# Kernel tuning notes

Measured on AMD Instinct MI355X. Metric: run time of the kernel, lower is better.

The kernel has to match this reference:

```python
import jax, jax.numpy as jnp
import numpy as np

B, C = 32768, 1000
ALPHA, P, BETA = 0.5, 2.0, 0.3
E1, E2 = 60, 80
MAGIC = 0.165745444183859  # constant subtracted from max_m in __init__


def setup_inputs() -> dict:
    key = jax.random.key(0)
    k1, k2, k3, k4 = jax.random.split(key, 4)
    x = jax.random.normal(k1, (B, C), dtype=jnp.float32)
    targets = jax.random.randint(k2, (B,), 0, C)
    # per-class sample counts (long-tailed): positive floats in [5, 1280]
    cls_num_list = jax.random.uniform(k3, (C,), dtype=jnp.float32, minval=5.0, maxval=1280.0)
    class_difficulty = jax.random.uniform(k4, (C,), dtype=jnp.float32)
    return {"x": x, "targets": targets, "cls_num_list": cls_num_list,
            "class_difficulty": class_difficulty, "epoch": 70}


def reference(x, targets, cls_num_list, class_difficulty, epoch):
    # ---- margins from class frequency (computed in __init__) ----
    max_m = -jnp.log(jnp.min(cls_num_list) / jnp.sum(cls_num_list)) - MAGIC
    cls_p = 1.0 / jnp.sqrt(cls_num_list)          # [C]
    m_list = max_m * cls_p / jnp.max(cls_p)       # [C]
    # ---- difficulty-based weights ----
    weights = ALPHA * class_difficulty ** P + BETA
    weights = weights * (max_m / jnp.max(weights))
    # ---- epoch schedule (epoch is a static Python int) ----
    if epoch < E1:
        m_list1 = m_list
    else:
        ee = 1.0 if epoch >= E2 else (epoch - E1) / (E2 - E1)
        m_list1 = m_list + weights * ee / 2
    # ---- subtract per-sample margin only at the target logit ----
    batch_m = m_list1[targets]                    # [B], == matmul(m_list1, onehot.T)
    rows = jnp.arange(B)
    output = x.at[rows, targets].add(-batch_m)    # torch.where(index, x - batch_m, x)
    # ---- safe_cross_entropy with s=1.0 (s kwarg not passed at call site) ----
    log_probs = jax.nn.log_softmax(output * 1.0, axis=1)
    loss = -jnp.mean(log_probs[rows, targets])
    return loss
```

## Files before the change

### kernel.cpp

```cpp
#include <hip/hip_runtime.h>
#include <math.h>

#define B_SZ 32768
#define C_SZ 1000
#define NV4  250

typedef float fvec4 __attribute__((ext_vector_type(4)));

__constant__ float kMAGIC = 0.165745444183859f;

__global__ void prep_kernel(const float* __restrict__ cls,
                            const float* __restrict__ diff,
                            const int*   __restrict__ epoch_p,
                            float*       __restrict__ m1) {
    __shared__ float smin[256], ssum[256], smax[256];
    const int tid = threadIdx.x;
    float mn = INFINITY, sm = 0.f, mx = -INFINITY;
    for (int c = tid; c < C_SZ; c += 256) {
        float v = cls[c];
        mn = fminf(mn, v);
        sm += v;
        mx = fmaxf(mx, diff[c]);
    }
    smin[tid] = mn; ssum[tid] = sm; smax[tid] = mx;
    __syncthreads();
    for (int s = 128; s > 0; s >>= 1) {
        if (tid < s) {
            smin[tid] = fminf(smin[tid], smin[tid + s]);
            ssum[tid] += ssum[tid + s];
            smax[tid] = fmaxf(smax[tid], smax[tid + s]);
        }
        __syncthreads();
    }
    __shared__ float sh_maxm, sh_minc, sh_wsc, sh_ee2;
    if (tid == 0) {
        const float minc = smin[0], sumc = ssum[0], maxd = smax[0];
        const float maxm = -logf(minc / sumc) - kMAGIC;
        const float maxw = 0.5f * maxd * maxd + 0.3f;
        const int epoch = epoch_p[0];
        float ee2;
        if (epoch < 60)       ee2 = 0.f;
        else if (epoch >= 80) ee2 = 0.5f;
        else                  ee2 = 0.5f * (float)(epoch - 60) / 20.0f;
        sh_maxm = maxm; sh_minc = minc; sh_wsc = maxm / maxw; sh_ee2 = ee2;
    }
    __syncthreads();
    const float maxm = sh_maxm, minc = sh_minc, wsc = sh_wsc, ee2 = sh_ee2;
    for (int c = tid; c < C_SZ; c += 256) {
        const float w = (0.5f * diff[c] * diff[c] + 0.3f) * wsc;
        m1[c] = maxm * sqrtf(minc / cls[c]) + w * ee2;
    }
}

__global__ __launch_bounds__(256) void loss_kernel(const float* __restrict__ x,
                                                   const int*   __restrict__ targets,
                                                   const float* __restrict__ m1,
                                                   float*       __restrict__ partials) {
    const int lane = threadIdx.x & 63;
    const int wv   = threadIdx.x >> 6;
    const int gw   = blockIdx.x * 4 + wv;
    const int nw   = gridDim.x * 4;

    float acc = 0.f;
    for (int row = gw; row < B_SZ; row += nw) {
        const fvec4* __restrict__ xr = (const fvec4*)(x + (size_t)row * C_SZ);
        const int   t  = targets[row];
        const float bm = m1[t];

        fvec4 v[4];
        #pragma unroll
        for (int k = 0; k < 4; ++k) {
            const int i4 = lane + 64 * k;
            if (i4 < NV4) v[k] = __builtin_nontemporal_load(&xr[i4]);
            else          v[k] = (fvec4){0.f, 0.f, 0.f, 0.f};
        }

        float s = 0.f;
        #pragma unroll
        for (int k = 0; k < 4; ++k) {
            const int i4   = lane + 64 * k;
            const int base = i4 * 4;
            if (i4 < NV4) {
                s += __expf(v[k].x - ((t == base + 0) ? bm : 0.f));
                s += __expf(v[k].y - ((t == base + 1) ? bm : 0.f));
                s += __expf(v[k].z - ((t == base + 2) ? bm : 0.f));
                s += __expf(v[k].w - ((t == base + 3) ? bm : 0.f));
            }
        }
        #pragma unroll
        for (int off = 32; off > 0; off >>= 1)
            s += __shfl_xor(s, off);

        const float xt = x[(size_t)row * C_SZ + t] - bm;
        acc += __logf(s) - xt;
    }

    __shared__ float sw[4];
    if (lane == 0) sw[wv] = acc;
    __syncthreads();
    if (threadIdx.x == 0)
        partials[blockIdx.x] = sw[0] + sw[1] + sw[2] + sw[3];
}

__global__ void finish_kernel(const float* __restrict__ partials, int n,
                              float* __restrict__ out) {
    __shared__ float sh[256];
    const int tid = threadIdx.x;
    float s = 0.f;
    for (int i = tid; i < n; i += 256) s += partials[i];
    sh[tid] = s;
    __syncthreads();
    for (int k = 128; k > 0; k >>= 1) {
        if (tid < k) sh[tid] += sh[tid + k];
        __syncthreads();
    }
    if (tid == 0) out[0] = sh[0] / (float)B_SZ;
}

extern "C" void kernel_launch(void* const* d_in, const int* in_sizes, int n_in,
                              void* d_out, int out_size, void* d_ws, size_t ws_size,
                              hipStream_t stream) {
    const float* x       = (const float*)d_in[0];
    const int*   targets = (const int*)d_in[1];
    const float* cls     = (const float*)d_in[2];
    const float* diff    = (const float*)d_in[3];
    const int*   epoch   = (const int*)d_in[4];
    float*       out     = (float*)d_out;

    float* m1       = (float*)d_ws;
    float* partials = m1 + C_SZ;

    prep_kernel<<<1, 256, 0, stream>>>(cls, diff, epoch, m1);

    const int grid = 2048;
    loss_kernel<<<grid, 256, 0, stream>>>(x, targets, m1, partials);

    finish_kernel<<<1, 256, 0, stream>>>(partials, grid, out);
}
```

Before: 195.4 us.

## Map one wave per row, drop per-element margin selects, launch full grid

Replaces the grid-stride row loop with one wave per row and a grid of B/4 blocks, so each block handles four rows with no loop. The target-logit margin is no longer applied element by element; the plain exp sum is corrected afterwards by swapping exp(xt) for exp(xt-bm). Padding lanes now use -1e9, and loads are ordinary cached loads instead of nontemporal ones. Launch bounds raise requested occupancy. The subtractive correction can lose precision when the target logit dominates the sum, and the finish kernel now reduces 8192 partials instead of 2048.

```diff
diff --git a/kernel.cpp b/kernel.cpp
--- a/kernel.cpp
+++ b/kernel.cpp
@@ -52,51 +52,43 @@
     }
 }
 
-__global__ __launch_bounds__(256) void loss_kernel(const float* __restrict__ x,
-                                                   const int*   __restrict__ targets,
-                                                   const float* __restrict__ m1,
-                                                   float*       __restrict__ partials) {
+__global__ __launch_bounds__(256, 8) void loss_kernel(const float* __restrict__ x,
+                                                      const int*   __restrict__ targets,
+                                                      const float* __restrict__ m1,
+                                                      float*       __restrict__ partials) {
     const int lane = threadIdx.x & 63;
     const int wv   = threadIdx.x >> 6;
-    const int gw   = blockIdx.x * 4 + wv;
-    const int nw   = gridDim.x * 4;
+    const int row  = blockIdx.x * 4 + wv;
 
-    float acc = 0.f;
-    for (int row = gw; row < B_SZ; row += nw) {
-        const fvec4* __restrict__ xr = (const fvec4*)(x + (size_t)row * C_SZ);
-        const int   t  = targets[row];
-        const float bm = m1[t];
+    const int   t  = targets[row];
+    const float bm = m1[t];
+    const float xt = x[(size_t)row * C_SZ + t];
 
-        fvec4 v[4];
-        #pragma unroll
-        for (int k = 0; k < 4; ++k) {
-            const int i4 = lane + 64 * k;
-            if (i4 < NV4) v[k] = __builtin_nontemporal_load(&xr[i4]);
-            else          v[k] = (fvec4){0.f, 0.f, 0.f, 0.f};
-        }
+    const fvec4* __restrict__ xr = (const fvec4*)(x + (size_t)row * C_SZ);
 
-        float s = 0.f;
-        #pragma unroll
-        for (int k = 0; k < 4; ++k) {
-            const int i4   = lane + 64 * k;
-            const int base = i4 * 4;
-            if (i4 < NV4) {
-                s += __expf(v[k].x - ((t == base + 0) ? bm : 0.f));
-                s += __expf(v[k].y - ((t == base + 1) ? bm : 0.f));
-                s += __expf(v[k].z - ((t == base + 2) ? bm : 0.f));
-                s += __expf(v[k].w - ((t == base + 3) ? bm : 0.f));
-            }
-        }
-        #pragma unroll
-        for (int off = 32; off > 0; off >>= 1)
-            s += __shfl_xor(s, off);
-
-        const float xt = x[(size_t)row * C_SZ + t] - bm;
-        acc += __logf(s) - xt;
+    fvec4 v[4];
+    #pragma unroll
+    for (int k = 0; k < 4; ++k) {
+        const int i4 = lane + 64 * k;
+        if (i4 < NV4) v[k] = xr[i4];
+        else          v[k] = (fvec4){-1e9f, -1e9f, -1e9f, -1e9f};
     }
 
+    float s = 0.f;
+    #pragma unroll
+    for (int k = 0; k < 4; ++k)
+        s += __expf(v[k].x) + __expf(v[k].y) + __expf(v[k].z) + __expf(v[k].w);
+
+    #pragma unroll
+    for (int off = 32; off > 0; off >>= 1)
+        s += __shfl_xor(s, off);
+
     __shared__ float sw[4];
-    if (lane == 0) sw[wv] = acc;
+    if (lane == 0) {
+        const float xtm   = xt - bm;
+        const float denom = s - __expf(xt) + __expf(xtm);
+        sw[wv] = __logf(denom) - xtm;
+    }
     __syncthreads();
     if (threadIdx.x == 0)
         partials[blockIdx.x] = sw[0] + sw[1] + sw[2] + sw[3];
@@ -132,7 +124,7 @@
 
     prep_kernel<<<1, 256, 0, stream>>>(cls, diff, epoch, m1);
 
-    const int grid = 2048;
+    const int grid = B_SZ / 4;
     loss_kernel<<<grid, 256, 0, stream>>>(x, targets, m1, partials);
 
     finish_kernel<<<1, 256, 0, stream>>>(partials, grid, out);
```

Result: slower. 201.9 us (+3.3%).
